# Performance work log

Measured on AMD Instinct MI355X. Metric: run time of the kernel, lower is better.

## Reference

```python
import jax, jax.numpy as jnp
import numpy as np
import math

B, CIN, CH, H, W = 4, 64, 32, 64, 64
M_CH, DEPTH, K = 4, 3, 8
NPF = CIN // 2  # num_pos_feats per axis; pos channels = 2*NPF = CIN
TEMPERATURE = 10000.0


def sine_pos(h, w, npf, temperature=TEMPERATURE):
    # PositionEmbeddingSine with normalize=False; cumsum of ones == arange(1, n+1)
    y_embed = jnp.arange(1, h + 1, dtype=jnp.float32)
    x_embed = jnp.arange(1, w + 1, dtype=jnp.float32)
    dim_t = jnp.arange(npf, dtype=jnp.float32)
    dim_t = temperature ** (2.0 * jnp.floor(dim_t / 2.0) / npf)
    pos_x = jnp.broadcast_to(x_embed[None, :, None] / dim_t, (h, w, npf))
    pos_y = jnp.broadcast_to(y_embed[:, None, None] / dim_t, (h, w, npf))

    def interleave(p):
        return jnp.stack([jnp.sin(p[..., 0::2]), jnp.cos(p[..., 1::2])], axis=-1).reshape(h, w, npf)

    pos = jnp.concatenate([interleave(pos_y), interleave(pos_x)], axis=-1)  # (h,w,2*npf)
    return jnp.transpose(pos, (2, 0, 1))  # (2*npf, h, w)


def conv2d(x, wgt, bias, pad):
    y = jax.lax.conv_general_dilated(
        x, wgt, window_strides=(1, 1), padding=[(pad, pad), (pad, pad)],
        dimension_numbers=('NCHW', 'OIHW', 'NCHW'))
    return y + bias[None, :, None, None]


def setup_inputs() -> dict:
    key = jax.random.key(0)
    ks = jax.random.split(key, 13)
    s = 0.05
    return {
        'f':    jax.random.normal(ks[0], (B, CH, H, W), jnp.float32),
        'map':  jax.random.normal(ks[1], (B, 1, 32, 32), jnp.float32),
        'f_q':  jax.random.normal(ks[2], (B, CIN, H, W), jnp.float32),
        'f_k':  jax.random.normal(ks[3], (B, CIN, H, W), jnp.float32),
        'm_k':  jax.random.normal(ks[4], (B, 1, 32, 32), jnp.float32),
        'wq':   jax.random.normal(ks[5], (M_CH, CIN), jnp.float32) * s,
        'wk':   jax.random.normal(ks[6], (M_CH, CIN), jnp.float32) * s,
        'w_in':  jax.random.normal(ks[7], (CH, CH, 1, 1), jnp.float32) * s,
        'b_in':  jax.random.normal(ks[8], (CH,), jnp.float32) * s,
        'w_mid': jax.random.normal(ks[9], (DEPTH, CH, CH, 3, 3), jnp.float32) * s,
        'b_mid': jax.random.normal(ks[10], (DEPTH, CH), jnp.float32) * s,
        'w_out': jax.random.normal(ks[11], (1, CH, 3, 3), jnp.float32) * s,
        'b_out': jax.random.normal(ks[12], (1,), jnp.float32) * s,
    }


def reference(f, map, f_q, f_k, m_k, wq, wk, w_in, b_in, w_mid, b_mid, w_out, b_out):
    b, c, h, w = f_q.shape
    hf, wf = f.shape[2], f.shape[3]
    # self.ret: bilinear resize to f's spatial size (align_corners=False)
    map_r = jax.image.resize(map, (b, 1, hf, wf), method='bilinear')
    m_k_r = jax.image.resize(m_k, (b, 1, hf, wf), method='bilinear')

    pos = sine_pos(h, w, NPF)[None]  # (1, CIN, h, w); same for pos_emb_h/pos_emb_l
    fq_emb = f_q + pos
    fk_emb = f_k + pos

    # 1x1 convs == channel matmuls
    query = jnp.einsum('mc,bchw->bhwm', wq, fq_emb).reshape(b, h * w, M_CH)  # (b, N, m)
    key_t = jnp.einsum('mc,bchw->bmhw', wk, fk_emb).reshape(b, M_CH, h * w)  # (b, m, N)

    sim = jnp.einsum('bqm,bmk->bqk', query, key_t)   # (b, N, N)
    sim = jax.nn.softmax(sim, axis=-2)                # softmax over query axis (dim=-2)

    value = (jnp.exp(m_k_r) / math.e).reshape(b, 1, h * w)  # broadcast over query axis
    context = sim * value
    context_k, _ = jax.lax.top_k(context, K)          # (b, N, K) over last (key) axis
    context_m = jnp.mean(context_k, axis=-1)          # (b, N)
    corrected_map = context_m.reshape(b, 1, h, w)

    corrected_map = corrected_map * map_r + map_r
    rmap = 1.0 - jax.nn.sigmoid(corrected_map)

    x = rmap * f  # broadcast over channel dim
    x = conv2d(x, w_in, b_in, 0)
    for i in range(DEPTH):
        x = jax.nn.relu(conv2d(x, w_mid[i], b_mid[i], 1))
    out = conv2d(x, w_out, b_out, 1) + corrected_map
    return (x, out, corrected_map)
```

## Files before the change

kernel.cpp:

```cpp
#include <hip/hip_runtime.h>
#include <hip/hip_bf16.h>
#include <math.h>

#define BB 4
#define CIN 64
#define CH 32
#define HH 64
#define WW 64
#define NN 4096
#define MCH 4
#define NQCH 32
#define LOG2E 1.4426950408889634f

#define PP_OFF     0
#define Q4_OFF     1024
#define K4_OFF     66560
#define CV_OFF     132096
#define CPMAX_OFF  148480
#define CPSUM_OFF  672768
#define RMAP_OFF   148480
#define CMAPF_OFF  164864
#define XA_OFF     181248
#define XB_OFF     705536

#define OUT_X_OFF   0
#define OUT_O_OFF   524288
#define OUT_CM_OFF  540672

__device__ __forceinline__ float bilin32(const float* src, int b, int y, int x) {
    float sy = 0.5f * y - 0.25f;
    float sx = 0.5f * x - 0.25f;
    float fy0 = floorf(sy), fx0 = floorf(sx);
    int y0 = (int)fy0, x0 = (int)fx0;
    float fy = sy - fy0, fx = sx - fx0;
    int y0c = min(max(y0, 0), 31), y1c = min(max(y0 + 1, 0), 31);
    int x0c = min(max(x0, 0), 31), x1c = min(max(x0 + 1, 0), 31);
    const float* p = src + b * 1024;
    float v00 = p[y0c * 32 + x0c], v01 = p[y0c * 32 + x1c];
    float v10 = p[y1c * 32 + x0c], v11 = p[y1c * 32 + x1c];
    float v0 = v00 + fx * (v01 - v00);
    float v1 = v10 + fx * (v11 - v10);
    return v0 + fy * (v1 - v0);
}

__global__ void k0_posproj(const float* __restrict__ wq, const float* __restrict__ wk,
                           float* __restrict__ pp) {
    int t = threadIdx.x;
    float coord = (float)(t + 1);
    float qy[4] = {0,0,0,0}, qx[4] = {0,0,0,0}, ky[4] = {0,0,0,0}, kx[4] = {0,0,0,0};
    for (int c = 0; c < 32; ++c) {
        float e = (2.0f * (float)(c / 2)) / 32.0f;
        float dim = powf(10000.0f, e);
        float ang = coord / dim;
        float pr = (c & 1) ? cosf(ang) : sinf(ang);
        #pragma unroll
        for (int m = 0; m < 4; ++m) {
            qy[m] += wq[m * 64 + c] * pr;
            qx[m] += wq[m * 64 + 32 + c] * pr;
            ky[m] += wk[m * 64 + c] * pr;
            kx[m] += wk[m * 64 + 32 + c] * pr;
        }
    }
    #pragma unroll
    for (int m = 0; m < 4; ++m) {
        pp[0 * 256 + m * 64 + t] = qy[m];
        pp[1 * 256 + m * 64 + t] = qx[m];
        pp[2 * 256 + m * 64 + t] = ky[m];
        pp[3 * 256 + m * 64 + t] = kx[m];
    }
}

__global__ void k1_qk(const float* __restrict__ fq, const float* __restrict__ fk,
                      const float* __restrict__ wq, const float* __restrict__ wk,
                      const float* __restrict__ pp,
                      float* __restrict__ Q4, float* __restrict__ K4) {
    __shared__ float wqs[256], wks[256];
    __shared__ float red[256][9];
    int tid = threadIdx.x;
    wqs[tid] = wq[tid];
    wks[tid] = wk[tid];
    __syncthreads();
    int qi = tid & 63, g = tid >> 6;
    int gid = blockIdx.x * 64 + qi;
    int b = gid >> 12, hw = gid & 4095;
    const float* fqb = fq + (size_t)b * CIN * NN + hw;
    const float* fkb = fk + (size_t)b * CIN * NN + hw;
    float aq[4] = {0,0,0,0}, ak[4] = {0,0,0,0};
    int c0 = g * 16;
    #pragma unroll 4
    for (int c = c0; c < c0 + 16; ++c) {
        float vq = fqb[c * NN];
        float vk = fkb[c * NN];
        #pragma unroll
        for (int m = 0; m < 4; ++m) {
            aq[m] += wqs[m * 64 + c] * vq;
            ak[m] += wks[m * 64 + c] * vk;
        }
    }
    #pragma unroll
    for (int m = 0; m < 4; ++m) { red[tid][m] = aq[m]; red[tid][4 + m] = ak[m]; }
    __syncthreads();
    if (tid < 64) {
        int y = hw >> 6, x = hw & 63;
        float q4[4], k4[4];
        #pragma unroll
        for (int m = 0; m < 4; ++m) {
            q4[m] = LOG2E * (red[tid][m] + red[tid + 64][m] + red[tid + 128][m] + red[tid + 192][m]
                  + pp[0 * 256 + m * 64 + y] + pp[1 * 256 + m * 64 + x]);
            k4[m] = red[tid][4 + m] + red[tid + 64][4 + m] + red[tid + 128][4 + m] + red[tid + 192][4 + m]
                  + pp[2 * 256 + m * 64 + y] + pp[3 * 256 + m * 64 + x];
        }
        ((float4*)Q4)[gid] = make_float4(q4[0], q4[1], q4[2], q4[3]);
        ((float4*)K4)[gid] = make_float4(k4[0], k4[1], k4[2], k4[3]);
    }
}

__global__ void k2a_colstats(const float* __restrict__ Q4, const float* __restrict__ K4,
                             float* __restrict__ cpsum) {
    __shared__ float4 Qs[128];
    int blk = blockIdx.x;
    int kblk = blk & 7;   blk >>= 3;
    int qch  = blk & 31;  blk >>= 5;
    int b    = blk;
    int tid = threadIdx.x;
    if (tid < 128)
        Qs[tid] = ((const float4*)Q4)[b * NN + qch * 128 + tid];
    __syncthreads();
    int k0 = kblk * 512 + tid;
    float4 kva = ((const float4*)K4)[b * NN + k0];
    float4 kvb = ((const float4*)K4)[b * NN + k0 + 256];
    float sa = 0.0f, sb = 0.0f;
    #pragma unroll 8
    for (int i = 0; i < 128; ++i) {
        float4 q = Qs[i];
        float da = fmaf(q.x, kva.x, fmaf(q.y, kva.y, fmaf(q.z, kva.z, q.w * kva.w)));
        float db = fmaf(q.x, kvb.x, fmaf(q.y, kvb.y, fmaf(q.z, kvb.z, q.w * kvb.w)));
        sa += exp2f(da);
        sb += exp2f(db);
    }
    cpsum[(b * NQCH + qch) * NN + k0] = sa;
    cpsum[(b * NQCH + qch) * NN + k0 + 256] = sb;
}

__global__ void k2b_cmerge(const float* __restrict__ cpsum,
                           const float* __restrict__ m_k, float* __restrict__ cvals) {
    int gid = blockIdx.x * 256 + threadIdx.x;
    int b = gid >> 12, k = gid & 4095;
    float S = 0.0f;
    #pragma unroll
    for (int j = 0; j < NQCH; ++j) S += cpsum[(b * NQCH + j) * NN + k];
    float mk = bilin32(m_k, b, k >> 6, k & 63);
    cvals[gid] = LOG2E * (mk - 1.0f) - log2f(S);
}

__global__ __launch_bounds__(256, 4) void k3_top8(
        const float* __restrict__ Q4, const float* __restrict__ K4,
        const float* __restrict__ cvals, const float* __restrict__ mapin,
        float* __restrict__ rmap, float* __restrict__ cmapf,
        float* __restrict__ outp) {
    int blk = blockIdx.x;
    int b = blk >> 10;
    int qbase = (blk & 1023) * 4;
    int tid = threadIdx.x;
    int wave = tid >> 6;
    int lane = tid & 63;
    int q = qbase + wave;
    float4 qv = ((const float4*)Q4)[b * NN + q];
    const float4* Kb = (const float4*)K4 + b * NN;
    const float* cb = cvals + b * NN;

    float sv[64];
    float mx = -1e30f;
    #pragma unroll
    for (int i = 0; i < 64; ++i) {
        int k = i * 64 + lane;
        float4 kv = Kb[k];
        float s = fmaf(qv.x, kv.x, fmaf(qv.y, kv.y,
                  fmaf(qv.z, kv.z, fmaf(qv.w, kv.w, cb[k]))));
        sv[i] = s;
        mx = fmaxf(mx, s);
    }

    float gmax = mx;
    gmax = fmaxf(gmax, __shfl_xor(gmax, 1));
    gmax = fmaxf(gmax, __shfl_xor(gmax, 2));
    gmax = fmaxf(gmax, __shfl_xor(gmax, 4));
    float T = gmax;
    T = fminf(T, __shfl_xor(T, 8));
    T = fminf(T, __shfl_xor(T, 16));
    T = fminf(T, __shfl_xor(T, 32));

    float t0 = -1e30f, t1 = -1e30f, t2 = -1e30f, t3 = -1e30f;
    float t4 = -1e30f, t5 = -1e30f, t6 = -1e30f, t7 = -1e30f;
    #pragma unroll
    for (int i = 0; i < 64; ++i) {
        float s = sv[i];
        if (s >= T && s > t0) {
            float a = fmaxf(t0, s);
            t0 = fminf(a, t1); a = fmaxf(a, t1);
            t1 = fminf(a, t2); a = fmaxf(a, t2);
            t2 = fminf(a, t3); a = fmaxf(a, t3);
            t3 = fminf(a, t4); a = fmaxf(a, t4);
            t4 = fminf(a, t5); a = fmaxf(a, t5);
            t5 = fminf(a, t6); a = fmaxf(a, t6);
            t6 = fminf(a, t7); t7 = fmaxf(a, t7);
        }
    }

    float sm = 0.0f;
    #pragma unroll
    for (int r = 0; r < 8; ++r) {
        float v = t7;
        int ln = lane;
        #pragma unroll
        for (int off = 32; off >= 1; off >>= 1) {
            float ov = __shfl_xor(v, off);
            int ol = __shfl_xor(ln, off);
            if (ov > v || (ov == v && ol < ln)) { v = ov; ln = ol; }
        }
        sm += exp2f(v);
        if (lane == ln) {
            t7 = t6; t6 = t5; t5 = t4; t4 = t3; t3 = t2; t2 = t1; t1 = t0; t0 = -1e30f;
        }
    }

    if (lane == 0) {
        float cmv = sm * 0.125f;
        int gid = b * NN + q;
        float mr = bilin32(mapin, b, q >> 6, q & 63);
        float cm = cmv * mr + mr;
        float rm = 1.0f / (1.0f + __expf(cm));
        rmap[gid] = rm;
        cmapf[gid] = cm;
        outp[OUT_CM_OFF + gid] = cm;
    }
}

__global__ void k4_conv1(const float* __restrict__ f, const float* __restrict__ rmap,
                         const float* __restrict__ w_in, const float* __restrict__ b_in,
                         float* __restrict__ xout) {
    __shared__ float ws_[1024];
    __shared__ float bs[32];
    int tid = threadIdx.x;
    for (int i = tid; i < 1024; i += 256) ws_[i] = w_in[i];
    if (tid < 32) bs[tid] = b_in[tid];
    __syncthreads();
    int gid = blockIdx.x * 256 + tid;
    int hw = gid & 4095;
    int og = (gid >> 12) & 7;
    int b  = gid >> 15;
    float rm = rmap[b * NN + hw];
    float acc[4];
    #pragma unroll
    for (int j = 0; j < 4; ++j) acc[j] = bs[og * 4 + j];
    const float* fb = f + (size_t)b * CH * NN + hw;
    for (int i = 0; i < 32; ++i) {
        float v = fb[i * NN] * rm;
        #pragma unroll
        for (int j = 0; j < 4; ++j) acc[j] += ws_[(og * 4 + j) * 32 + i] * v;
    }
    float* xo = xout + (size_t)b * CH * NN + (og * 4) * NN + hw;
    #pragma unroll
    for (int j = 0; j < 4; ++j) xo[j * NN] = acc[j];
}

__global__ void k5_conv3(const float* __restrict__ xin, const float* __restrict__ w,
                         const float* __restrict__ bias, float* __restrict__ xout,
                         float* __restrict__ outx) {
    __shared__ float tile[32][324];
    __shared__ float wsm[1152];
    __shared__ float bsm[4];
    int blk = blockIdx.x;
    int og = blk & 7;  blk >>= 3;
    int tx = blk & 3;  blk >>= 2;
    int ty = blk & 3;  blk >>= 2;
    int b  = blk;
    int tid = threadIdx.x;
    for (int i = tid; i < 1152; i += 256) wsm[i] = w[og * 1152 + i];
    if (tid < 4) bsm[tid] = bias[og * 4 + tid];
    int y0 = ty * 16 - 1, x0 = tx * 16 - 1;
    for (int i = tid; i < 32 * 324; i += 256) {
        int c = i / 324, r = i % 324;
        int yy = r / 18, xx = r % 18;
        int gy = y0 + yy, gx = x0 + xx;
        float v = 0.0f;
        if (gy >= 0 && gy < 64 && gx >= 0 && gx < 64)
            v = xin[((size_t)b * CH + c) * NN + gy * 64 + gx];
        tile[c][r] = v;
    }
    __syncthreads();
    int py = tid >> 4, px = tid & 15;
    float acc[4];
    #pragma unroll
    for (int j = 0; j < 4; ++j) acc[j] = bsm[j];
    for (int i = 0; i < 32; ++i) {
        const float* tr = &tile[i][py * 18 + px];
        float v00 = tr[0],  v01 = tr[1],  v02 = tr[2];
        float v10 = tr[18], v11 = tr[19], v12 = tr[20];
        float v20 = tr[36], v21 = tr[37], v22 = tr[38];
        #pragma unroll
        for (int j = 0; j < 4; ++j) {
            const float* wj = &wsm[j * 288 + i * 9];
            acc[j] += v00 * wj[0] + v01 * wj[1] + v02 * wj[2]
                    + v10 * wj[3] + v11 * wj[4] + v12 * wj[5]
                    + v20 * wj[6] + v21 * wj[7] + v22 * wj[8];
        }
    }
    size_t base = (size_t)b * CH * NN + (size_t)(og * 4) * NN
                + (ty * 16 + py) * 64 + tx * 16 + px;
    #pragma unroll
    for (int j = 0; j < 4; ++j) {
        float r_ = fmaxf(acc[j], 0.0f);
        xout[base + j * NN] = r_;
        if (outx) outx[base + j * NN] = r_;
    }
}

__global__ void k6_convout(const float* __restrict__ xin, const float* __restrict__ w_out,
                           const float* __restrict__ b_out, const float* __restrict__ cmapf,
                           float* __restrict__ outp) {
    __shared__ float wsm[288];
    __shared__ float red[256];
    int tid = threadIdx.x;
    for (int i = tid; i < 288; i += 256) wsm[i] = w_out[i];
    int pxi = tid & 63, g = tid >> 6;
    int gid = blockIdx.x * 64 + pxi;
    int b = gid >> 12, hw = gid & 4095;
    int y = hw >> 6, x = hw & 63;
    __syncthreads();
    float acc = 0.0f;
    int c0 = g * 8;
    for (int i = c0; i < c0 + 8; ++i) {
        const float* xi = xin + ((size_t)b * CH + i) * NN;
        #pragma unroll
        for (int ky = 0; ky < 3; ++ky) {
            int gy = y + ky - 1;
            if (gy < 0 || gy > 63) continue;
            #pragma unroll
            for (int kx = 0; kx < 3; ++kx) {
                int gx = x + kx - 1;
                if (gx < 0 || gx > 63) continue;
                acc += xi[gy * 64 + gx] * wsm[i * 9 + ky * 3 + kx];
            }
        }
    }
    red[tid] = acc;
    __syncthreads();
    if (tid < 64) {
        float a = red[tid] + red[tid + 64] + red[tid + 128] + red[tid + 192]
                + b_out[0] + cmapf[gid];
        outp[OUT_O_OFF + gid] = a;
    }
}

extern "C" void kernel_launch(void* const* d_in, const int* in_sizes, int n_in,
                              void* d_out, int out_size, void* d_ws, size_t ws_size,
                              hipStream_t stream) {
    const float* f     = (const float*)d_in[0];
    const float* mapin = (const float*)d_in[1];
    const float* f_q   = (const float*)d_in[2];
    const float* f_k   = (const float*)d_in[3];
    const float* m_k   = (const float*)d_in[4];
    const float* wq    = (const float*)d_in[5];
    const float* wk    = (const float*)d_in[6];
    const float* w_in  = (const float*)d_in[7];
    const float* b_in  = (const float*)d_in[8];
    const float* w_mid = (const float*)d_in[9];
    const float* b_mid = (const float*)d_in[10];
    const float* w_out = (const float*)d_in[11];
    const float* b_out = (const float*)d_in[12];
    float* outp = (float*)d_out;
    float* ws = (float*)d_ws;

    float* PP    = ws + PP_OFF;
    float* Q4    = ws + Q4_OFF;
    float* K4    = ws + K4_OFF;
    float* CV    = ws + CV_OFF;
    float* CPSUM = ws + CPSUM_OFF;
    float* RMAP  = ws + RMAP_OFF;
    float* CMAPF = ws + CMAPF_OFF;
    float* XA    = ws + XA_OFF;
    float* XB    = ws + XB_OFF;

    k0_posproj<<<1, 64, 0, stream>>>(wq, wk, PP);
    k1_qk<<<256, 256, 0, stream>>>(f_q, f_k, wq, wk, PP, Q4, K4);
    k2a_colstats<<<BB * NQCH * 8, 256, 0, stream>>>(Q4, K4, CPSUM);
    k2b_cmerge<<<64, 256, 0, stream>>>(CPSUM, m_k, CV);
    k3_top8<<<BB * 1024, 256, 0, stream>>>(Q4, K4, CV, mapin, RMAP, CMAPF, outp);
    k4_conv1<<<512, 256, 0, stream>>>(f, RMAP, w_in, b_in, XA);
    k5_conv3<<<512, 256, 0, stream>>>(XA, w_mid + 0 * 9216, b_mid + 0 * 32, XB, (float*)0);
    k5_conv3<<<512, 256, 0, stream>>>(XB, w_mid + 1 * 9216, b_mid + 1 * 32, XA, (float*)0);
    k5_conv3<<<512, 256, 0, stream>>>(XA, w_mid + 2 * 9216, b_mid + 2 * 32, XB, outp + OUT_X_OFF);
    k6_convout<<<256, 256, 0, stream>>>(XB, w_out, b_out, CMAPF, outp);
}
```

Before: 224.8 us.

## Split top-8 into per-thread LDS-tiled key scan plus wave merge

Replaces the one-query-per-wave top-8 kernel with two kernels. In the first, each thread owns one query and scans a 512-key chunk of K and the column values staged in shared memory, keeping a running top-8 and writing eight candidates per chunk. In the second, one wave per query merges the 64 candidates and applies the map/sigmoid epilogue. This removes the repeated global/L2 reads of K for every query and the per-query wave-wide threshold reductions. In exchange it adds a 4 MB intermediate buffer (overlapping the later XA/XB buffers), an extra launch, and divergent insertion branches in a long serial per-thread loop.

```diff
diff --git a/kernel.cpp b/kernel.cpp
--- a/kernel.cpp
+++ b/kernel.cpp
@@ -16,10 +16,10 @@
 #define Q4_OFF     1024
 #define K4_OFF     66560
 #define CV_OFF     132096
-#define CPMAX_OFF  148480
 #define CPSUM_OFF  672768
 #define RMAP_OFF   148480
 #define CMAPF_OFF  164864
+#define T8_OFF     181248
 #define XA_OFF     181248
 #define XB_OFF     705536
 
@@ -153,49 +153,36 @@
     cvals[gid] = LOG2E * (mk - 1.0f) - log2f(S);
 }
 
-__global__ __launch_bounds__(256, 4) void k3_top8(
-        const float* __restrict__ Q4, const float* __restrict__ K4,
-        const float* __restrict__ cvals, const float* __restrict__ mapin,
-        float* __restrict__ rmap, float* __restrict__ cmapf,
-        float* __restrict__ outp) {
+__global__ void k3a_scan(const float* __restrict__ Q4, const float* __restrict__ K4,
+                         const float* __restrict__ cvals, float* __restrict__ t8) {
+    __shared__ float4 kvs[512];
+    __shared__ float  cvs[512];
     int blk = blockIdx.x;
-    int b = blk >> 10;
-    int qbase = (blk & 1023) * 4;
-    int tid = threadIdx.x;
-    int wave = tid >> 6;
-    int lane = tid & 63;
-    int q = qbase + wave;
-    float4 qv = ((const float4*)Q4)[b * NN + q];
-    const float4* Kb = (const float4*)K4 + b * NN;
-    const float* cb = cvals + b * NN;
-
-    float sv[64];
-    float mx = -1e30f;
-    #pragma unroll
-    for (int i = 0; i < 64; ++i) {
-        int k = i * 64 + lane;
-        float4 kv = Kb[k];
-        float s = fmaf(qv.x, kv.x, fmaf(qv.y, kv.y,
-                  fmaf(qv.z, kv.z, fmaf(qv.w, kv.w, cb[k]))));
-        sv[i] = s;
-        mx = fmaxf(mx, s);
-    }
-
-    float gmax = mx;
-    gmax = fmaxf(gmax, __shfl_xor(gmax, 1));
-    gmax = fmaxf(gmax, __shfl_xor(gmax, 2));
-    gmax = fmaxf(gmax, __shfl_xor(gmax, 4));
-    float T = gmax;
-    T = fminf(T, __shfl_xor(T, 8));
-    T = fminf(T, __shfl_xor(T, 16));
-    T = fminf(T, __shfl_xor(T, 32));
-
+    int kc = blk & 7;   blk >>= 3;
+    int g2 = blk & 15;  blk >>= 4;
+    int b  = blk;
+    int tid = threadIdx.x;
+    int wave = tid >> 6, lane = tid & 63;
+
+    const float4* Kb = (const float4*)K4 + b * NN + kc * 512;
+    const float* cb = cvals + b * NN + kc * 512;
+    #pragma unroll
+    for (int i = tid; i < 512; i += 256) {
+        kvs[i] = Kb[i];
+        cvs[i] = cb[i];
+    }
+    __syncthreads();
+
+    int qrow = (g2 * 4 + wave) * 64 + lane;
+    float4 qv = ((const float4*)Q4)[b * NN + qrow];
     float t0 = -1e30f, t1 = -1e30f, t2 = -1e30f, t3 = -1e30f;
     float t4 = -1e30f, t5 = -1e30f, t6 = -1e30f, t7 = -1e30f;
-    #pragma unroll
-    for (int i = 0; i < 64; ++i) {
-        float s = sv[i];
-        if (s >= T && s > t0) {
+    #pragma unroll 4
+    for (int i = 0; i < 512; ++i) {
+        float4 kv = kvs[i];
+        float s = fmaf(qv.x, kv.x, fmaf(qv.y, kv.y,
+                  fmaf(qv.z, kv.z, fmaf(qv.w, kv.w, cvs[i]))));
+        if (s > t0) {
             float a = fmaxf(t0, s);
             t0 = fminf(a, t1); a = fmaxf(a, t1);
             t1 = fminf(a, t2); a = fmaxf(a, t2);
@@ -206,33 +193,41 @@
             t6 = fminf(a, t7); t7 = fmaxf(a, t7);
         }
     }
-
+    float* o = t8 + ((size_t)(b * NN + qrow)) * 64 + kc * 8;
+    o[0] = t0; o[1] = t1; o[2] = t2; o[3] = t3;
+    o[4] = t4; o[5] = t5; o[6] = t6; o[7] = t7;
+}
+
+__global__ void k3b_merge(const float* __restrict__ t8, const float* __restrict__ mapin,
+                          float* __restrict__ rmap, float* __restrict__ cmapf,
+                          float* __restrict__ outp) {
+    int tid = threadIdx.x;
+    int qid = blockIdx.x * 4 + (tid >> 6);
+    int lane = tid & 63;
+    float v = t8[(size_t)qid * 64 + lane];
     float sm = 0.0f;
     #pragma unroll
     for (int r = 0; r < 8; ++r) {
-        float v = t7;
+        float m = v;
         int ln = lane;
         #pragma unroll
         for (int off = 32; off >= 1; off >>= 1) {
-            float ov = __shfl_xor(v, off);
+            float om = __shfl_xor(m, off);
             int ol = __shfl_xor(ln, off);
-            if (ov > v || (ov == v && ol < ln)) { v = ov; ln = ol; }
-        }
-        sm += exp2f(v);
-        if (lane == ln) {
-            t7 = t6; t6 = t5; t5 = t4; t4 = t3; t3 = t2; t2 = t1; t1 = t0; t0 = -1e30f;
-        }
-    }
-
+            if (om > m || (om == m && ol < ln)) { m = om; ln = ol; }
+        }
+        sm += exp2f(m);
+        if (lane == ln) v = -1e30f;
+    }
     if (lane == 0) {
         float cmv = sm * 0.125f;
-        int gid = b * NN + q;
-        float mr = bilin32(mapin, b, q >> 6, q & 63);
+        int b = qid >> 12, hw = qid & 4095;
+        float mr = bilin32(mapin, b, hw >> 6, hw & 63);
         float cm = cmv * mr + mr;
         float rm = 1.0f / (1.0f + __expf(cm));
-        rmap[gid] = rm;
-        cmapf[gid] = cm;
-        outp[OUT_CM_OFF + gid] = cm;
+        rmap[qid] = rm;
+        cmapf[qid] = cm;
+        outp[OUT_CM_OFF + qid] = cm;
     }
 }
 
@@ -379,6 +374,7 @@
     float* CPSUM = ws + CPSUM_OFF;
     float* RMAP  = ws + RMAP_OFF;
     float* CMAPF = ws + CMAPF_OFF;
+    float* T8    = ws + T8_OFF;
     float* XA    = ws + XA_OFF;
     float* XB    = ws + XB_OFF;
 
@@ -386,7 +382,8 @@
     k1_qk<<<256, 256, 0, stream>>>(f_q, f_k, wq, wk, PP, Q4, K4);
     k2a_colstats<<<BB * NQCH * 8, 256, 0, stream>>>(Q4, K4, CPSUM);
     k2b_cmerge<<<64, 256, 0, stream>>>(CPSUM, m_k, CV);
-    k3_top8<<<BB * 1024, 256, 0, stream>>>(Q4, K4, CV, mapin, RMAP, CMAPF, outp);
+    k3a_scan<<<BB * 16 * 8, 256, 0, stream>>>(Q4, K4, CV, T8);
+    k3b_merge<<<BB * NN / 4, 256, 0, stream>>>(T8, mapin, RMAP, CMAPF, outp);
     k4_conv1<<<512, 256, 0, stream>>>(f, RMAP, w_in, b_in, XA);
     k5_conv3<<<512, 256, 0, stream>>>(XA, w_mid + 0 * 9216, b_mid + 0 * 32, XB, (float*)0);
     k5_conv3<<<512, 256, 0, stream>>>(XB, w_mid + 1 * 9216, b_mid + 1 * 32, XA, (float*)0);
```

Result: slower. 235.5 us (+4.7%).
